# Kernel optimization log

Measured on AMD Instinct MI355X. Metric: run time of the kernel, lower is better.

The kernel has to match this reference:

```python
import jax, jax.numpy as jnp
import numpy as np

B, T, C, HD = 4, 4096, 1024, 64

def setup_inputs() -> dict:
    key = jax.random.key(0)
    k1, k2, k3, k4 = jax.random.split(key, 4)
    x = jax.random.normal(k1, (B, T, C), dtype=jnp.float32)
    scale = 1.0 / np.sqrt(C)
    Wq = jax.random.normal(k2, (C, HD), dtype=jnp.float32) * scale
    Wk = jax.random.normal(k3, (C, HD), dtype=jnp.float32) * scale
    Wv = jax.random.normal(k4, (C, HD), dtype=jnp.float32) * scale
    return {"x": x, "Wq": Wq, "Wk": Wk, "Wv": Wv}

def reference(x, Wq, Wk, Wv):
    # q,k,v: [B,T,HD]
    q = jnp.einsum('btc,ch->bth', x, Wq)
    k = jnp.einsum('btc,ch->bth', x, Wk)
    v = jnp.einsum('btc,ch->bth', x, Wv)
    hd = q.shape[-1]
    scores = jnp.einsum('bth,bsh->bts', q, k) / jnp.sqrt(jnp.float32(hd))  # [B,T,T]
    causal = jnp.tril(jnp.ones((scores.shape[1], scores.shape[1]), dtype=bool))
    scores = jnp.where(causal, scores, -jnp.inf)
    attn = jax.nn.softmax(scores, axis=-1)
    return jnp.einsum('bts,bsh->bth', attn, v)  # [B,T,HD]
```

## Files before the change

### kernel.cpp

```cpp
#include <hip/hip_runtime.h>
#include <hip/hip_bf16.h>

typedef __attribute__((ext_vector_type(8))) short bf16x8;
typedef __attribute__((ext_vector_type(4))) short bf16x4;
typedef __attribute__((ext_vector_type(4))) float f32x4;
typedef __attribute__((ext_vector_type(4))) int   i32x4;

#define C2LOG 0.18033688011112042f
#define THR_RAW 44.3616f

__device__ __forceinline__ short f2bf(float f) {
    union { float f; unsigned u; } v; v.f = f;
    unsigned r = v.u + 0x7fff + ((v.u >> 16) & 1);
    return (short)(r >> 16);
}
__device__ __forceinline__ unsigned cvtpk(float lo, float hi) {
    unsigned r;
    asm("v_cvt_pk_bf16_f32 %0, %1, %2" : "=v"(r) : "v"(lo), "v"(hi));
    return r;
}
__device__ __forceinline__ float bf2f(short s) {
    union { unsigned u; float f; } v; v.u = ((unsigned)(unsigned short)s) << 16;
    return v.f;
}

#define BB 4
#define TT 4096
#define CC 1024
#define HD 64
#define NTASK_PB 144
#define NTASK (BB * NTASK_PB)

__global__ __launch_bounds__(256) void prep_w(const float* __restrict__ Wq,
        const float* __restrict__ Wk, const float* __restrict__ Wv,
        short* __restrict__ Wt) {
    __shared__ float wls[64][65];
    const int w = blockIdx.x >> 4;
    const int c = blockIdx.x & 15;
    const float* W = (w == 0) ? Wq : (w == 1) ? Wk : Wv;

    const int r  = threadIdx.x >> 4;
    const int q4 = threadIdx.x & 15;
    #pragma unroll
    for (int rr = 0; rr < 4; ++rr) {
        const int row = rr * 16 + r;
        float4 v = *reinterpret_cast<const float4*>(
            W + (size_t)(c * 64 + row) * HD + q4 * 4);
        wls[row][q4 * 4 + 0] = v.x;
        wls[row][q4 * 4 + 1] = v.y;
        wls[row][q4 * 4 + 2] = v.z;
        wls[row][q4 * 4 + 3] = v.w;
    }
    __syncthreads();

    const int n  = threadIdx.x >> 2;
    const int ks = (threadIdx.x & 3) * 16;
    bf16x8 o0, o1;
    #pragma unroll
    for (int j = 0; j < 8; ++j) o0[j] = f2bf(wls[ks + j][n]);
    #pragma unroll
    for (int j = 0; j < 8; ++j) o1[j] = f2bf(wls[ks + 8 + j][n]);
    short* dst = Wt + (size_t)(w * 64 + n) * CC + c * 64 + ks;
    *reinterpret_cast<bf16x8*>(dst)     = o0;
    *reinterpret_cast<bf16x8*>(dst + 8) = o1;
}

__global__ __launch_bounds__(512) void proj_qkv(const float* __restrict__ x,
        const short* __restrict__ Wt, short* __restrict__ Q,
        short* __restrict__ K, short* __restrict__ Vt) {
    __shared__ short xs[2][32 * 72];
    __shared__ short wsm[2][192 * 64];

    const int tid  = threadIdx.x;
    const int lane = tid & 63;
    const int wv   = tid >> 6;
    const int lm   = lane & 15;
    const int lg   = lane >> 4;
    const int mhalf = wv & 1;
    const int ngrp  = wv >> 1;
    const int mbase = blockIdx.x * 32;

    const int xr  = tid >> 4;
    const int xq4 = tid & 15;
    const float* xrow = x + (size_t)(mbase + xr) * CC;

    int wsrow[3], wscol[3];
    #pragma unroll
    for (int it = 0; it < 3; ++it) {
        const int off = it * 8192 + wv * 1024 + lane * 16;
        wsrow[it] = off >> 7;
        wscol[it] = (off & 127) ^ ((wsrow[it] & 7) << 4);
    }

#define STAGE_W(bufidx, kc)                                                           \
    {                                                                                 \
        _Pragma("unroll")                                                             \
        for (int it = 0; it < 3; ++it) {                                              \
            const char* src = (const char*)(Wt + (size_t)wsrow[it] * CC + (kc) * 64)  \
                              + wscol[it];                                            \
            char* dst = (char*)&wsm[bufidx][0] + it * 8192 + wv * 1024;               \
            __builtin_amdgcn_global_load_lds(                                         \
                (const __attribute__((address_space(1))) unsigned*)src,               \
                (__attribute__((address_space(3))) unsigned*)dst, 16, 0, 0);          \
        }                                                                             \
    }

#define CONV_X(bufidx, xv)                                                            \
    {                                                                                 \
        int2 pk;                                                                      \
        pk.x = (int)cvtpk((xv).x, (xv).y);                                            \
        pk.y = (int)cvtpk((xv).z, (xv).w);                                            \
        *reinterpret_cast<int2*>(&xs[bufidx][xr * 72 + xq4 * 4]) = pk;                \
    }

    f32x4 acc[3];
    #pragma unroll
    for (int i = 0; i < 3; ++i) acc[i] = f32x4{0.f, 0.f, 0.f, 0.f};

    {
        float4 v = *reinterpret_cast<const float4*>(xrow + xq4 * 4);
        CONV_X(0, v)
        STAGE_W(0, 0)
    }
    asm volatile("s_waitcnt vmcnt(0)" ::: "memory");
    __syncthreads();

    const int arow = mhalf * 16 + lm;
    int buf = 0;
    for (int kc = 0; kc < 16; ++kc) {
        float4 nv;
        const bool more = (kc < 15);
        if (more) {
            nv = *reinterpret_cast<const float4*>(xrow + (kc + 1) * 64 + xq4 * 4);
            STAGE_W(buf ^ 1, kc + 1)
        }

        bf16x8 a0 = *reinterpret_cast<const bf16x8*>(&xs[buf][arow * 72 + lg * 8]);
        bf16x8 a1 = *reinterpret_cast<const bf16x8*>(&xs[buf][arow * 72 + 32 + lg * 8]);
        #pragma unroll
        for (int c = 0; c < 3; ++c) {
            const int brow = (ngrp * 3 + c) * 16 + lm;
            const int sw = (brow & 7) << 4;
            bf16x8 b0 = *reinterpret_cast<const bf16x8*>(
                (const char*)&wsm[buf][0] + brow * 128 + ((lg * 16) ^ sw));
            bf16x8 b1 = *reinterpret_cast<const bf16x8*>(
                (const char*)&wsm[buf][0] + brow * 128 + ((64 + lg * 16) ^ sw));
            acc[c] = __builtin_amdgcn_mfma_f32_16x16x32_bf16(a0, b0, acc[c], 0, 0, 0);
            acc[c] = __builtin_amdgcn_mfma_f32_16x16x32_bf16(a1, b1, acc[c], 0, 0, 0);
        }

        if (more) CONV_X(buf ^ 1, nv)
        asm volatile("s_waitcnt vmcnt(0)" ::: "memory");
        __syncthreads();
        buf ^= 1;
    }
#undef STAGE_W
#undef CONV_X

    const int mrow = mbase + mhalf * 16 + lg * 4;
    #pragma unroll
    for (int c = 0; c < 3; ++c) {
        const int cn = ngrp * 3 + c;
        if (cn < 4) {
            #pragma unroll
            for (int r = 0; r < 4; ++r)
                Q[(size_t)(mrow + r) * HD + cn * 16 + lm] = f2bf(acc[c][r]);
        } else if (cn < 8) {
            #pragma unroll
            for (int r = 0; r < 4; ++r)
                K[(size_t)(mrow + r) * HD + (cn - 4) * 16 + lm] = f2bf(acc[c][r]);
        } else {
            const int bb   = mbase >> 12;
            const int tloc = (mbase & 4095) + mhalf * 16 + lg * 4;
            int2 pk;
            pk.x = (int)cvtpk(acc[c][0], acc[c][1]);
            pk.y = (int)cvtpk(acc[c][2], acc[c][3]);
            *reinterpret_cast<int2*>(
                Vt + (size_t)bb * (HD * TT) + (size_t)((cn - 8) * 16 + lm) * TT + tloc) = pk;
        }
    }
}

__global__ __launch_bounds__(256, 3) void attn(const short* __restrict__ Q,
        const short* __restrict__ K, const short* __restrict__ Vt,
        short* __restrict__ Opart, float* __restrict__ Mpart,
        float* __restrict__ Lpart) {
    __shared__ short ks[3][64 * 64];
    __shared__ short vs[3][64 * 64];

    const int tid  = threadIdx.x;
    const int lane = tid & 63;
    const int wv   = tid >> 6;
    const int lm   = lane & 15;
    const int lg   = lane >> 4;

    const int task = blockIdx.x;
    const int b  = task / NTASK_PB;
    int t_in = task - b * NTASK_PB;
    int g = 0;
    while (t_in >= 2 * (g + 1) * (g + 2)) ++g;
    const int idx = t_in - 2 * g * (g + 1);
    const int i   = 4 * g + idx / (g + 1);
    const int seg = idx % (g + 1);
    const int S   = g + 1;
    const int niter = 2 * i + 2;
    const int nloop = (niter - seg + S - 1) / S;

    const size_t qkb = (size_t)b * TT * HD;
    const size_t vtb = (size_t)b * HD * TT;
    const int qrow = i * 128 + wv * 32;
    const int tmax = (qrow + 31) >> 6;

    bf16x8 qf0 = *reinterpret_cast<const bf16x8*>(Q + qkb + (size_t)(qrow + lm) * HD + lg * 8);
    bf16x8 qf1 = *reinterpret_cast<const bf16x8*>(Q + qkb + (size_t)(qrow + lm) * HD + 32 + lg * 8);
    bf16x8 qf2 = *reinterpret_cast<const bf16x8*>(Q + qkb + (size_t)(qrow + 16 + lm) * HD + lg * 8);
    bf16x8 qf3 = *reinterpret_cast<const bf16x8*>(Q + qkb + (size_t)(qrow + 16 + lm) * HD + 32 + lg * 8);

    f32x4 oA[4], oB[4];
    #pragma unroll
    for (int c = 0; c < 4; ++c) { oA[c] = f32x4{0.f,0.f,0.f,0.f}; oB[c] = f32x4{0.f,0.f,0.f,0.f}; }
    float mrunA = -1e30f, lrunA = 0.f;
    float mrunB = -1e30f, lrunB = 0.f;

    const int srcA = lm + ((lane & 16) << 1);
    const int srcB = srcA + 16;
    const bool hihalf = (lane & 32) != 0;

    int srow[2], scol[2];
    #pragma unroll
    for (int c = 0; c < 2; ++c) {
        const int off = wv * 2048 + c * 1024 + lane * 16;
        srow[c] = off >> 7;
        scol[c] = (off & 127) ^ ((srow[c] & 7) << 4);
    }

#define STAGE_KV(bufidx, tt)                                                          \
    {                                                                                 \
        _Pragma("unroll")                                                             \
        for (int c = 0; c < 2; ++c) {                                                 \
            const char* ksrc = (const char*)(K + qkb) + (tt) * 8192                   \
                               + (srow[c] << 7) + scol[c];                            \
            char* kdst = (char*)&ks[bufidx][0] + wv * 2048 + c * 1024;                \
            __builtin_amdgcn_global_load_lds(                                         \
                (const __attribute__((address_space(1))) unsigned*)ksrc,              \
                (__attribute__((address_space(3))) unsigned*)kdst, 16, 0, 0);         \
            const char* vsrc = (const char*)(Vt + vtb) + (size_t)srow[c] * (TT * 2)   \
                               + (tt) * 128 + scol[c];                                \
            char* vdst = (char*)&vs[bufidx][0] + wv * 2048 + c * 1024;                \
            __builtin_amdgcn_global_load_lds(                                         \
                (const __attribute__((address_space(1))) unsigned*)vsrc,              \
                (__attribute__((address_space(3))) unsigned*)vdst, 16, 0, 0);         \
        }                                                                             \
    }

    STAGE_KV(0, seg)
    if (nloop > 1) {
        STAGE_KV(1, seg + S)
        asm volatile("s_waitcnt vmcnt(4)" ::: "memory");
    } else {
        asm volatile("s_waitcnt vmcnt(0)" ::: "memory");
    }
    __builtin_amdgcn_s_barrier();

    for (int n = 0; n < nloop; ++n) {
        const int t = seg + n * S;
        const bool stage2 = (n + 2 < nloop);
        if (stage2) STAGE_KV((n + 2) % 3, t + 2 * S)

        if (t <= tmax) {
            const short* ksb = &ks[n % 3][0];
            const short* vsb = &vs[n % 3][0];
            const int kv = t * 64;

            f32x4 stA[4], stB[4];
            #pragma unroll
            for (int kt = 0; kt < 4; ++kt) {
                const int krow = kt * 16 + lm;
                const int sw = (krow & 7) << 4;
                bf16x8 k0 = *reinterpret_cast<const bf16x8*>(
                    (const char*)ksb + krow * 128 + ((lg * 16) ^ sw));
                bf16x8 k1 = *reinterpret_cast<const bf16x8*>(
                    (const char*)ksb + krow * 128 + ((64 + lg * 16) ^ sw));
                f32x4 a = f32x4{0.f,0.f,0.f,0.f};
                a = __builtin_amdgcn_mfma_f32_16x16x32_bf16(k0, qf0, a, 0, 0, 0);
                a = __builtin_amdgcn_mfma_f32_16x16x32_bf16(k1, qf1, a, 0, 0, 0);
                stA[kt] = a;
                f32x4 bb2 = f32x4{0.f,0.f,0.f,0.f};
                bb2 = __builtin_amdgcn_mfma_f32_16x16x32_bf16(k0, qf2, bb2, 0, 0, 0);
                bb2 = __builtin_amdgcn_mfma_f32_16x16x32_bf16(k1, qf3, bb2, 0, 0, 0);
                stB[kt] = bb2;
            }

            if (kv + 63 > qrow) {
                const int qgA = qrow + lm;
                const int qgB = qrow + 16 + lm;
                #pragma unroll
                for (int kt = 0; kt < 4; ++kt)
                    #pragma unroll
                    for (int r = 0; r < 4; ++r) {
                        const int kk = kv + kt * 16 + lg * 4 + r;
                        if (kk > qgA) stA[kt][r] = -1e30f;
                        if (kk > qgB) stB[kt][r] = -1e30f;
                    }
            }

            float mA0 = fmaxf(fmaxf(stA[0][0], stA[0][1]), fmaxf(stA[0][2], stA[0][3]));
            float mA1 = fmaxf(fmaxf(stA[1][0], stA[1][1]), fmaxf(stA[1][2], stA[1][3]));
            float mA2 = fmaxf(fmaxf(stA[2][0], stA[2][1]), fmaxf(stA[2][2], stA[2][3]));
            float mA3 = fmaxf(fmaxf(stA[3][0], stA[3][1]), fmaxf(stA[3][2], stA[3][3]));
            float mlocA = fmaxf(fmaxf(mA0, mA1), fmaxf(mA2, mA3));
            float mB0 = fmaxf(fmaxf(stB[0][0], stB[0][1]), fmaxf(stB[0][2], stB[0][3]));
            float mB1 = fmaxf(fmaxf(stB[1][0], stB[1][1]), fmaxf(stB[1][2], stB[1][3]));
            float mB2 = fmaxf(fmaxf(stB[2][0], stB[2][1]), fmaxf(stB[2][2], stB[2][3]));
            float mB3 = fmaxf(fmaxf(stB[3][0], stB[3][1]), fmaxf(stB[3][2], stB[3][3]));
            float mlocB = fmaxf(fmaxf(mB0, mB1), fmaxf(mB2, mB3));
            mlocA = fmaxf(mlocA, __shfl_xor(mlocA, 16));
            mlocA = fmaxf(mlocA, __shfl_xor(mlocA, 32));
            mlocB = fmaxf(mlocB, __shfl_xor(mlocB, 16));
            mlocB = fmaxf(mlocB, __shfl_xor(mlocB, 32));

            if (!__all(mlocA <= mrunA + THR_RAW)) {
                const float mnewA = fmaxf(mrunA, mlocA);
                const float alphaA = __builtin_amdgcn_exp2f((mrunA - mnewA) * C2LOG);
                mrunA = mnewA;
                lrunA *= alphaA;
                #pragma unroll
                for (int c = 0; c < 4; ++c)
                    #pragma unroll
                    for (int r = 0; r < 4; ++r) oA[c][r] *= alphaA;
            }
            if (!__all(mlocB <= mrunB + THR_RAW)) {
                const float mnewB = fmaxf(mrunB, mlocB);
                const float alphaB = __builtin_amdgcn_exp2f((mrunB - mnewB) * C2LOG);
                mrunB = mnewB;
                lrunB *= alphaB;
                #pragma unroll
                for (int c = 0; c < 4; ++c)
                    #pragma unroll
                    for (int r = 0; r < 4; ++r) oB[c][r] *= alphaB;
            }

            const float ncA = -mrunA * C2LOG;
            const float ncB = -mrunB * C2LOG;
            float pA[4][4], pB[4][4];
            float rsA = 0.f, rsB = 0.f;
            #pragma unroll
            for (int kt = 0; kt < 4; ++kt)
                #pragma unroll
                for (int r = 0; r < 4; ++r) {
                    pA[kt][r] = __builtin_amdgcn_exp2f(__builtin_fmaf(stA[kt][r], C2LOG, ncA));
                    rsA += pA[kt][r];
                    pB[kt][r] = __builtin_amdgcn_exp2f(__builtin_fmaf(stB[kt][r], C2LOG, ncB));
                    rsB += pB[kt][r];
                }
            rsA += __shfl_xor(rsA, 16); rsA += __shfl_xor(rsA, 32);
            rsB += __shfl_xor(rsB, 16); rsB += __shfl_xor(rsB, 32);
            lrunA += rsA;
            lrunB += rsB;

            unsigned uA[4][2], uB[4][2];
            #pragma unroll
            for (int kt = 0; kt < 4; ++kt) {
                uA[kt][0] = cvtpk(pA[kt][0], pA[kt][1]);
                uA[kt][1] = cvtpk(pA[kt][2], pA[kt][3]);
                uB[kt][0] = cvtpk(pB[kt][0], pB[kt][1]);
                uB[kt][1] = cvtpk(pB[kt][2], pB[kt][3]);
            }

            #pragma unroll
            for (int h = 0; h < 2; ++h) {
                const int a0 = __shfl((int)uA[2*h][0],   srcA);
                const int a1c = __shfl((int)uA[2*h+1][0], srcA);
                const int a2 = __shfl((int)uA[2*h][1],   srcA);
                const int a3c = __shfl((int)uA[2*h+1][1], srcA);
                const int a4 = __shfl((int)uA[2*h][0],   srcB);
                const int a5c = __shfl((int)uA[2*h+1][0], srcB);
                const int a6 = __shfl((int)uA[2*h][1],   srcB);
                const int a7c = __shfl((int)uA[2*h+1][1], srcB);
                union { i32x4 iv; bf16x8 v; } cvA;
                cvA.iv = i32x4{ hihalf ? a1c : a0, hihalf ? a3c : a2,
                                hihalf ? a5c : a4, hihalf ? a7c : a6 };
                const int b0 = __shfl((int)uB[2*h][0],   srcA);
                const int b1c = __shfl((int)uB[2*h+1][0], srcA);
                const int b2 = __shfl((int)uB[2*h][1],   srcA);
                const int b3c = __shfl((int)uB[2*h+1][1], srcA);
                const int b4 = __shfl((int)uB[2*h][0],   srcB);
                const int b5c = __shfl((int)uB[2*h+1][0], srcB);
                const int b6 = __shfl((int)uB[2*h][1],   srcB);
                const int b7c = __shfl((int)uB[2*h+1][1], srcB);
                union { i32x4 iv; bf16x8 v; } cvB;
                cvB.iv = i32x4{ hihalf ? b1c : b0, hihalf ? b3c : b2,
                                hihalf ? b5c : b4, hihalf ? b7c : b6 };
                #pragma unroll
                for (int c = 0; c < 4; ++c) {
                    const int vrow = c * 16 + lm;
                    const int sw = (vrow & 7) << 4;
                    bf16x8 va = *reinterpret_cast<const bf16x8*>(
                        (const char*)vsb + vrow * 128 + ((h * 64 + lg * 16) ^ sw));
                    oA[c] = __builtin_amdgcn_mfma_f32_16x16x32_bf16(va, cvA.v, oA[c], 0, 0, 0);
                    oB[c] = __builtin_amdgcn_mfma_f32_16x16x32_bf16(va, cvB.v, oB[c], 0, 0, 0);
                }
            }
        }

        __builtin_amdgcn_sched_barrier(0);
        asm volatile("s_waitcnt lgkmcnt(0)" ::: "memory");
        if (stage2) asm volatile("s_waitcnt vmcnt(4)" ::: "memory");
        else        asm volatile("s_waitcnt vmcnt(0)" ::: "memory");
        __builtin_amdgcn_s_barrier();
    }
#undef STAGE_KV

    short* Ob = Opart + (size_t)task * (128 * HD);
    #pragma unroll
    for (int c = 0; c < 4; ++c) {
        int2 pkA, pkB;
        pkA.x = (int)cvtpk(oA[c][0], oA[c][1]);
        pkA.y = (int)cvtpk(oA[c][2], oA[c][3]);
        pkB.x = (int)cvtpk(oB[c][0], oB[c][1]);
        pkB.y = (int)cvtpk(oB[c][2], oB[c][3]);
        *reinterpret_cast<int2*>(&Ob[(wv * 32 + lm) * HD + c * 16 + lg * 4]) = pkA;
        *reinterpret_cast<int2*>(&Ob[(wv * 32 + 16 + lm) * HD + c * 16 + lg * 4]) = pkB;
    }
    if (lg == 0) {
        Mpart[task * 128 + wv * 32 + lm] = mrunA;
        Lpart[task * 128 + wv * 32 + lm] = lrunA;
        Mpart[task * 128 + wv * 32 + 16 + lm] = mrunB;
        Lpart[task * 128 + wv * 32 + 16 + lm] = lrunB;
    }
}

__global__ __launch_bounds__(256) void combine(const short* __restrict__ Opart,
        const float* __restrict__ Mpart, const float* __restrict__ Lpart,
        float* __restrict__ out) {
    const int b   = blockIdx.x >> 8;
    const int rem = blockIdx.x & 255;
    const int i   = rem >> 3;
    const int rr  = rem & 7;
    const int g = i >> 2;
    const int S = g + 1;
    const int task0 = b * NTASK_PB + 2 * g * (g + 1) + (i - 4 * g) * (g + 1);
    const int qbase = i * 128;

    const int tid = threadIdx.x;
    const int row = rr * 16 + (tid >> 4);
    const int cb  = (tid & 15) << 2;

    float mmax = -1e30f;
    float ms[8];
    for (int s = 0; s < S; ++s) {
        ms[s] = Mpart[(task0 + s) * 128 + row];
        mmax = fmaxf(mmax, ms[s]);
    }
    float lsum = 0.f;
    float a0 = 0.f, a1 = 0.f, a2 = 0.f, a3 = 0.f;
    for (int s = 0; s < S; ++s) {
        const float w = __builtin_amdgcn_exp2f((ms[s] - mmax) * C2LOG);
        lsum += Lpart[(task0 + s) * 128 + row] * w;
        bf16x4 ov = *reinterpret_cast<const bf16x4*>(
            &Opart[((size_t)(task0 + s) * 128 + row) * HD + cb]);
        a0 += bf2f(ov[0]) * w;
        a1 += bf2f(ov[1]) * w;
        a2 += bf2f(ov[2]) * w;
        a3 += bf2f(ov[3]) * w;
    }
    const float inv = 1.0f / lsum;
    f32x4 res{ a0 * inv, a1 * inv, a2 * inv, a3 * inv };
    *reinterpret_cast<f32x4*>(
        &out[((size_t)b * TT + qbase + row) * HD + cb]) = res;
}

extern "C" void kernel_launch(void* const* d_in, const int* in_sizes, int n_in,
                              void* d_out, int out_size, void* d_ws, size_t ws_size,
                              hipStream_t stream) {
    const float* x  = (const float*)d_in[0];
    const float* Wq = (const float*)d_in[1];
    const float* Wk = (const float*)d_in[2];
    const float* Wv = (const float*)d_in[3];
    float* out = (float*)d_out;

    char* ws = (char*)d_ws;
    short* Wt    = (short*)(ws);
    short* Q     = (short*)(ws + 393216);
    short* K     = (short*)(ws + 2490368);
    short* Vt    = (short*)(ws + 4587520);
    short* Opart = (short*)(ws + 6684672);
    float* Mpart = (float*)(ws + 16121856);
    float* Lpart = (float*)(ws + 16416768);

    hipLaunchKernelGGL(prep_w,   dim3(48),    dim3(256), 0, stream, Wq, Wk, Wv, Wt);
    hipLaunchKernelGGL(proj_qkv, dim3(512),   dim3(512), 0, stream, x, Wt, Q, K, Vt);
    hipLaunchKernelGGL(attn,     dim3(NTASK), dim3(256), 0, stream, Q, K, Vt,
                       Opart, Mpart, Lpart);
    hipLaunchKernelGGL(combine,  dim3(1024),  dim3(256), 0, stream,
                       Opart, Mpart, Lpart, out);
}
```

Measured before the change: 66.74 us.

## Fuse split-KV combine into attention kernel via last-block atomic counter

Removes the separate combine kernel launch. Query tiles handled by a single segment write normalized fp32 output directly. For split tiles, the last finishing block, found with an atomic counter plus threadfence, merges the partials. This saves a kernel launch and a pass over the partials, but adds a memset, atomics, and a serial tail of combine work in the last blocks.

Result: slower. 185.2 us (+177.5%).

```diff
diff --git a/kernel.cpp b/kernel.cpp
--- a/kernel.cpp
+++ b/kernel.cpp
@@ -184,9 +184,11 @@
 __global__ __launch_bounds__(256, 3) void attn(const short* __restrict__ Q,
         const short* __restrict__ K, const short* __restrict__ Vt,
         short* __restrict__ Opart, float* __restrict__ Mpart,
-        float* __restrict__ Lpart) {
+        float* __restrict__ Lpart, float* __restrict__ out,
+        int* __restrict__ cnt) {
     __shared__ short ks[3][64 * 64];
     __shared__ short vs[3][64 * 64];
+    __shared__ int is_last;
 
     const int tid  = threadIdx.x;
     const int lane = tid & 63;
@@ -411,6 +413,21 @@
     }
 #undef STAGE_KV
 
+    if (S == 1) {
+        const float invA = 1.0f / lrunA;
+        const float invB = 1.0f / lrunB;
+        float* Orow = out + ((size_t)b * TT + i * 128) * HD;
+        #pragma unroll
+        for (int c = 0; c < 4; ++c) {
+            f32x4 ra, rb;
+            #pragma unroll
+            for (int r = 0; r < 4; ++r) { ra[r] = oA[c][r] * invA; rb[r] = oB[c][r] * invB; }
+            *reinterpret_cast<f32x4*>(&Orow[(size_t)(wv * 32 + lm) * HD + c * 16 + lg * 4]) = ra;
+            *reinterpret_cast<f32x4*>(&Orow[(size_t)(wv * 32 + 16 + lm) * HD + c * 16 + lg * 4]) = rb;
+        }
+        return;
+    }
+
     short* Ob = Opart + (size_t)task * (128 * HD);
     #pragma unroll
     for (int c = 0; c < 4; ++c) {
@@ -428,46 +445,44 @@
         Mpart[task * 128 + wv * 32 + 16 + lm] = mrunB;
         Lpart[task * 128 + wv * 32 + 16 + lm] = lrunB;
     }
-}
-
-__global__ __launch_bounds__(256) void combine(const short* __restrict__ Opart,
-        const float* __restrict__ Mpart, const float* __restrict__ Lpart,
-        float* __restrict__ out) {
-    const int b   = blockIdx.x >> 8;
-    const int rem = blockIdx.x & 255;
-    const int i   = rem >> 3;
-    const int rr  = rem & 7;
-    const int g = i >> 2;
-    const int S = g + 1;
-    const int task0 = b * NTASK_PB + 2 * g * (g + 1) + (i - 4 * g) * (g + 1);
-    const int qbase = i * 128;
-
-    const int tid = threadIdx.x;
-    const int row = rr * 16 + (tid >> 4);
-    const int cb  = (tid & 15) << 2;
-
-    float mmax = -1e30f;
-    float ms[8];
-    for (int s = 0; s < S; ++s) {
-        ms[s] = Mpart[(task0 + s) * 128 + row];
-        mmax = fmaxf(mmax, ms[s]);
-    }
-    float lsum = 0.f;
-    float a0 = 0.f, a1 = 0.f, a2 = 0.f, a3 = 0.f;
-    for (int s = 0; s < S; ++s) {
-        const float w = __builtin_amdgcn_exp2f((ms[s] - mmax) * C2LOG);
-        lsum += Lpart[(task0 + s) * 128 + row] * w;
-        bf16x4 ov = *reinterpret_cast<const bf16x4*>(
-            &Opart[((size_t)(task0 + s) * 128 + row) * HD + cb]);
-        a0 += bf2f(ov[0]) * w;
-        a1 += bf2f(ov[1]) * w;
-        a2 += bf2f(ov[2]) * w;
-        a3 += bf2f(ov[3]) * w;
-    }
-    const float inv = 1.0f / lsum;
-    f32x4 res{ a0 * inv, a1 * inv, a2 * inv, a3 * inv };
-    *reinterpret_cast<f32x4*>(
-        &out[((size_t)b * TT + qbase + row) * HD + cb]) = res;
+
+    __threadfence();
+    if (tid == 0) {
+        const int gid = (b << 5) + i;
+        is_last = (atomicAdd(&cnt[gid], 1) == S - 1);
+    }
+    __syncthreads();
+    if (!is_last) return;
+    __threadfence();
+
+    const int task0 = task - seg;
+    const int row0  = tid >> 4;
+    const int cb    = (tid & 15) << 2;
+    for (int rr = 0; rr < 8; ++rr) {
+        const int row = rr * 16 + row0;
+        float mmax = -1e30f;
+        float ms[8];
+        for (int s = 0; s < S; ++s) {
+            ms[s] = Mpart[(task0 + s) * 128 + row];
+            mmax = fmaxf(mmax, ms[s]);
+        }
+        float lsum = 0.f;
+        float a0 = 0.f, a1 = 0.f, a2 = 0.f, a3 = 0.f;
+        for (int s = 0; s < S; ++s) {
+            const float w = __builtin_amdgcn_exp2f((ms[s] - mmax) * C2LOG);
+            lsum += Lpart[(task0 + s) * 128 + row] * w;
+            bf16x4 ov = *reinterpret_cast<const bf16x4*>(
+                &Opart[((size_t)(task0 + s) * 128 + row) * HD + cb]);
+            a0 += bf2f(ov[0]) * w;
+            a1 += bf2f(ov[1]) * w;
+            a2 += bf2f(ov[2]) * w;
+            a3 += bf2f(ov[3]) * w;
+        }
+        const float inv = 1.0f / lsum;
+        f32x4 res{ a0 * inv, a1 * inv, a2 * inv, a3 * inv };
+        *reinterpret_cast<f32x4*>(
+            &out[((size_t)b * TT + i * 128 + row) * HD + cb]) = res;
+    }
 }
 
 extern "C" void kernel_launch(void* const* d_in, const int* in_sizes, int n_in,
@@ -487,11 +502,11 @@
     short* Opart = (short*)(ws + 6684672);
     float* Mpart = (float*)(ws + 16121856);
     float* Lpart = (float*)(ws + 16416768);
-
+    int*   cnt   = (int*)(ws + 16711680);
+
+    hipMemsetAsync(cnt, 0, 128 * sizeof(int), stream);
     hipLaunchKernelGGL(prep_w,   dim3(48),    dim3(256), 0, stream, Wq, Wk, Wv, Wt);
     hipLaunchKernelGGL(proj_qkv, dim3(512),   dim3(512), 0, stream, x, Wt, Q, K, Vt);
     hipLaunchKernelGGL(attn,     dim3(NTASK), dim3(256), 0, stream, Q, K, Vt,
-                       Opart, Mpart, Lpart);
-    hipLaunchKernelGGL(combine,  dim3(1024),  dim3(256), 0, stream,
-                       Opart, Mpart, Lpart, out);
-}
+                       Opart, Mpart, Lpart, out, cnt);
+}
```
